# Kernel optimization log

Measured on AMD Instinct MI355X. Metric: run time of the kernel, lower is better.

The kernel has to match this reference:

```python
import jax, jax.numpy as jnp
import numpy as np
import math

DIM = 147      # input feature dim
EMB = 64       # in_dim * head_cnt
M = 32         # int(EMB * kernel_ratio)
EPS_LN = 1e-5
EPS = 1e-8


def layer_norm(x, g, b, eps=EPS_LN):
    mu = jnp.mean(x, axis=-1, keepdims=True)
    var = jnp.mean(jnp.square(x - mu), axis=-1, keepdims=True)
    return (x - mu) * jax.lax.rsqrt(var + eps) * g + b


def prm_exp(x, W_rf):
    # x: [b, t, e], W_rf: [m, e]
    xd = 0.5 * jnp.sum(x * x, axis=-1, keepdims=True)        # [b, t, 1]
    wtx = jnp.einsum('bte,me->btm', x, W_rf)                  # [b, t, m]
    return jnp.exp(wtx - xd) / math.sqrt(M)


def setup_inputs() -> dict:
    key = jax.random.key(0)
    ks = jax.random.split(key, 16)
    B, T = 32, 3136
    s_in = 1.0 / math.sqrt(DIM)
    s_emb = 1.0 / math.sqrt(EMB)
    inp = {
        'x':      jax.random.normal(ks[0], (B, T, DIM), jnp.float32),
        'w_kqv':  jax.random.uniform(ks[1], (3 * EMB, DIM), jnp.float32, -s_in, s_in),
        'b_kqv':  jax.random.uniform(ks[2], (3 * EMB,), jnp.float32, -s_in, s_in),
        'w_proj': jax.random.uniform(ks[3], (EMB, EMB), jnp.float32, -s_emb, s_emb),
        'b_proj': jax.random.uniform(ks[4], (EMB,), jnp.float32, -s_emb, s_emb),
        'g1':     jnp.ones((DIM,), jnp.float32),
        'beta1':  jnp.zeros((DIM,), jnp.float32),
        'g2':     jnp.ones((EMB,), jnp.float32),
        'beta2':  jnp.zeros((EMB,), jnp.float32),
        'w_m1':   jax.random.uniform(ks[5], (EMB, EMB), jnp.float32, -s_emb, s_emb),
        'b_m1':   jax.random.uniform(ks[6], (EMB,), jnp.float32, -s_emb, s_emb),
        'w_m2':   jax.random.uniform(ks[7], (EMB, EMB), jnp.float32, -s_emb, s_emb),
        'b_m2':   jax.random.uniform(ks[8], (EMB,), jnp.float32, -s_emb, s_emb),
        # orthogonal random-feature matrix scaled by sqrt(m) (buffer 'w')
        'W_rf':   jnp.asarray(np.linalg.qr(np.random.RandomState(0).randn(EMB, EMB))[0][:M] * math.sqrt(M), jnp.float32),
    }
    return inp


def reference(x, w_kqv, b_kqv, w_proj, b_proj, g1, beta1, g2, beta2,
              w_m1, b_m1, w_m2, b_m2, W_rf):
    # --- single_attn(norm1(x)) ---
    xn = layer_norm(x, g1, beta1)
    kqv = xn @ w_kqv.T + b_kqv                                  # [b, t, 3e]
    k, q, v = jnp.split(kqv, 3, axis=-1)
    kp = prm_exp(k, W_rf)                                       # [b, t, m]
    qp = prm_exp(q, W_rf)                                       # [b, t, m]
    D = jnp.einsum('btm,bm->bt', qp, kp.sum(axis=1))[..., None]  # [b, t, 1]
    kptv = jnp.einsum('bte,btm->bem', v, kp)                    # [b, e, m]
    y = jnp.einsum('btm,bem->bte', qp, kptv) / (D + EPS)        # [b, t, e]
    y = v + (y @ w_proj.T + b_proj)                             # residual on v
    # --- y + mlp(norm2(y)) ---
    yn = layer_norm(y, g2, beta2)
    h = jax.nn.gelu(yn @ w_m1.T + b_m1, approximate=False)
    out = y + (h @ w_m2.T + b_m2)
    return out
```

## Files before the change

kernel.cpp:

```cpp
#include <hip/hip_runtime.h>
#include <hip/hip_bf16.h>

#define BB 32
#define TT 3136
#define DD 147
#define EE 64
#define MM 32
#define BT (BB*TT)

typedef __hip_bfloat16 bf16;
typedef __attribute__((ext_vector_type(8))) short s8v;
typedef __attribute__((ext_vector_type(4))) float f4v;

__device__ __forceinline__ float b2f(bf16 v){ return __bfloat162float(v); }
__device__ __forceinline__ bf16 f2b(float v){ return __float2bfloat16(v); }
__device__ __forceinline__ unsigned pack2(float a, float b){
  union { bf16 h[2]; unsigned u; } cv; cv.h[0]=f2b(a); cv.h[1]=f2b(b); return cv.u;
}

template<typename T>
__device__ __forceinline__ float cvt1(T v);
template<> __device__ __forceinline__ float cvt1<float>(float v){ return v; }
template<> __device__ __forceinline__ float cvt1<bf16>(bf16 v){ return __bfloat162float(v); }

__device__ __forceinline__ int bf16flag(const void* g1){
  return (*(const unsigned*)g1 == 0x3F803F80u) ? 1 : 0;
}

template<typename T>
__device__ void cvt_body(int idx,
    const T* wkqv, const T* bkqv, const T* Wrf, const T* wproj, const T* bproj,
    const T* g2, const T* be2, const T* wm1, const T* bm1, const T* wm2,
    const T* bm2, const T* g1, const T* be1,
    bf16* Bprep, bf16* WrfB, bf16* w0B, float* bprojF,
    float* g2F, float* be2F, bf16* w1B, float* bm1F, bf16* w2B,
    float* bm2F, float* c2F)
{
  if (idx < 30720){
    int n = idx/160, k = idx - n*160;
    Bprep[idx] = f2b(k < DD ? cvt1(wkqv[n*DD + k]) * cvt1(g1[k]) : 0.f);
    return;
  }
  idx -= 30720;
  if (idx < 2048){ WrfB[idx] = f2b(cvt1(Wrf[idx])); return; }
  idx -= 2048;
  if (idx < 4608){
    int e = idx/72, c = idx - e*72;
    w0B[idx] = f2b(c < 64 ? cvt1(wproj[e*64 + c]) : 0.f); return;
  }
  idx -= 4608;
  if (idx < 64){ bprojF[idx] = cvt1(bproj[idx]); return; }
  idx -= 64;
  if (idx < 64){ g2F[idx] = cvt1(g2[idx]); return; }
  idx -= 64;
  if (idx < 64){ be2F[idx] = cvt1(be2[idx]); return; }
  idx -= 64;
  if (idx < 4608){
    int e = idx/72, c = idx - e*72;
    w1B[idx] = f2b(c < 64 ? cvt1(wm1[e*64 + c]) : 0.f); return;
  }
  idx -= 4608;
  if (idx < 64){ bm1F[idx] = cvt1(bm1[idx]); return; }
  idx -= 64;
  if (idx < 4608){
    int e = idx/72, c = idx - e*72;
    w2B[idx] = f2b(c < 64 ? cvt1(wm2[e*64 + c]) : 0.f); return;
  }
  idx -= 4608;
  if (idx < 64){ bm2F[idx] = cvt1(bm2[idx]); return; }
  idx -= 64;
  if (idx < 192){
    float s = cvt1(bkqv[idx]);
    for (int k=0; k<DD; ++k)
      s = fmaf(cvt1(wkqv[idx*DD + k]), cvt1(be1[k]), s);
    c2F[idx] = s; return;
  }
}

__global__ void k_cvt(const void* wkqv, const void* bkqv, const void* Wrf,
    const void* wproj, const void* bproj, const void* g2, const void* be2,
    const void* wm1, const void* bm1, const void* wm2, const void* bm2,
    const void* g1, const void* be1,
    bf16* Bprep, bf16* WrfB, bf16* w0B, float* bprojF,
    float* g2F, float* be2F, bf16* w1B, float* bm1F, bf16* w2B,
    float* bm2F, float* c2F,
    float* __restrict__ kptvF, float* __restrict__ ksumF)
{
  int idx = blockIdx.x*256 + threadIdx.x;
  if (idx < 65536) kptvF[idx] = 0.f;
  if (idx < 1024)  ksumF[idx] = 0.f;
  if (bf16flag(g1))
    cvt_body<bf16>(idx, (const bf16*)wkqv, (const bf16*)bkqv, (const bf16*)Wrf,
      (const bf16*)wproj, (const bf16*)bproj, (const bf16*)g2, (const bf16*)be2,
      (const bf16*)wm1, (const bf16*)bm1, (const bf16*)wm2, (const bf16*)bm2,
      (const bf16*)g1, (const bf16*)be1,
      Bprep, WrfB, w0B, bprojF, g2F, be2F, w1B, bm1F, w2B, bm2F, c2F);
  else
    cvt_body<float>(idx, (const float*)wkqv, (const float*)bkqv, (const float*)Wrf,
      (const float*)wproj, (const float*)bproj, (const float*)g2, (const float*)be2,
      (const float*)wm1, (const float*)bm1, (const float*)wm2, (const float*)bm2,
      (const float*)g1, (const float*)be1,
      Bprep, WrfB, w0B, bprojF, g2F, be2F, w1B, bm1F, w2B, bm2F, c2F);
}

__global__ __launch_bounds__(256,4) void k_a2(
    const void* __restrict__ x, const void* __restrict__ g1,
    const bf16* __restrict__ Bprep, const float* __restrict__ c2F,
    const bf16* __restrict__ WrfB,
    bf16* __restrict__ qp, bf16* __restrict__ v,
    float* __restrict__ kptvF, float* __restrict__ ksumF)
{
  __shared__ __align__(16) char smem[21504];
  bf16* vT   = (bf16*)smem;
  bf16* kpT  = (bf16*)(smem + 9216);

  int tid = threadIdx.x;
  size_t t0 = (size_t)blockIdx.x*64;
  int b = blockIdx.x / 49;

  int tw = tid>>6, lane = tid&63, quad = lane>>4, r = lane&15;
  int tRow = tw*16 + quad*4;
  char* strip = smem + tw*5376;
  bf16* lin = (bf16*)strip;
  bf16* aS  = (bf16*)strip;
  bf16* kqW = (bf16*)strip;

  if (bf16flag(g1)){
    const uint4* xg = (const uint4*)((const bf16*)x + (t0 + (size_t)tw*16)*DD);
    uint4* xo = (uint4*)lin;
    #pragma unroll
    for (int k=0; k<5; ++k){
      int c = k*64 + lane;
      if (c < 294) xo[c] = xg[c];
    }
  } else {
    const float4* xg = (const float4*)((const float*)x + (t0 + (size_t)tw*16)*DD);
    uint2* xo = (uint2*)lin;
    #pragma unroll
    for (int k=0; k<10; ++k){
      int c = k*64 + lane;
      if (c < 588){
        float4 f = xg[c];
        uint2 u; u.x = pack2(f.x, f.y); u.y = pack2(f.z, f.w);
        xo[c] = u;
      }
    }
  }

  int ti = lane>>2, sl = lane&3;
  const bf16* srow = lin + ti*DD;
  float xv[37];
  float s1 = 0.f, s2 = 0.f;
  #pragma unroll
  for (int j=0; j<37; ++j){
    int e = sl + 4*j;
    float vx = (e < DD) ? b2f(srow[e]) : 0.f;
    xv[j] = vx;
    s1 += vx;
    s2 = fmaf(vx, vx, s2);
  }
  s1 += __shfl_xor(s1,1); s1 += __shfl_xor(s1,2);
  s2 += __shfl_xor(s2,1); s2 += __shfl_xor(s2,2);
  float mu  = s1 * (1.f/147.f);
  float var = s2 * (1.f/147.f) - mu*mu;
  float rn  = rsqrtf(var + 1e-5f);

  bf16* arow = aS + ti*168;
  #pragma unroll
  for (int j=0; j<37; ++j){
    int e = sl + 4*j;
    if (e < DD)       arow[e] = f2b((xv[j]-mu)*rn);
    else if (e == DD) arow[e] = f2b(0.f);
  }
  arow[148+sl] = f2b(0.f); arow[152+sl] = f2b(0.f); arow[156+sl] = f2b(0.f);

  f4v zero = {0.f,0.f,0.f,0.f};

  f4v acc[12];
  #pragma unroll
  for (int nt=0; nt<12; ++nt) acc[nt] = zero;
  const bf16* aBase = aS + r*168 + quad*8;
  const bf16* bBase = &Bprep[r*160 + quad*8];
  #pragma unroll 1
  for (int ks=0; ks<5; ++ks){
    s8v a = *((const s8v*)(aBase + ks*32));
    #pragma unroll
    for (int nt=0; nt<12; ++nt){
      s8v bw = *((const s8v*)(bBase + nt*16*160 + ks*32));
      acc[nt] = __builtin_amdgcn_mfma_f32_16x16x32_bf16(a, bw, acc[nt], 0,0,0);
    }
  }

  float c2v[12];
  #pragma unroll
  for (int nt=0; nt<12; ++nt) c2v[nt] = c2F[nt*16 + r];

  float vv[4][4];
  #pragma unroll
  for (int nt=8; nt<12; ++nt){
    #pragma unroll
    for (int reg=0; reg<4; ++reg){
      vv[nt-8][reg] = acc[nt][reg] + c2v[nt];
      v[(t0 + tRow + reg)*64 + (nt-8)*16 + r] = f2b(vv[nt-8][reg]);
    }
  }

  float kq[8][4];
  #pragma unroll
  for (int nt=0; nt<8; ++nt)
    #pragma unroll
    for (int reg=0; reg<4; ++reg)
      kq[nt][reg] = acc[nt][reg] + c2v[nt];

  #pragma unroll
  for (int nt=0; nt<8; ++nt)
    #pragma unroll
    for (int reg=0; reg<4; ++reg)
      kqW[(quad*4+reg)*136 + nt*16 + r] = f2b(kq[nt][reg]);

  float xdk[4], xdq[4];
  #pragma unroll
  for (int reg=0; reg<4; ++reg){
    float sk = 0.f, sq = 0.f;
    #pragma unroll
    for (int nt=0; nt<4; ++nt){
      sk = fmaf(kq[nt][reg],   kq[nt][reg],   sk);
      sq = fmaf(kq[nt+4][reg], kq[nt+4][reg], sq);
    }
    #pragma unroll
    for (int off=1; off<16; off<<=1){
      sk += __shfl_xor(sk, off);
      sq += __shfl_xor(sq, off);
    }
    xdk[reg] = 0.5f*sk;
    xdq[reg] = 0.5f*sq;
  }

  f4v accP[2] = {zero, zero}, accQ[2] = {zero, zero};
  #pragma unroll
  for (int ks=0; ks<2; ++ks){
    s8v ak = *((const s8v*)&kqW[r*136 + ks*32 + quad*8]);
    s8v aq = *((const s8v*)&kqW[r*136 + 64 + ks*32 + quad*8]);
    #pragma unroll
    for (int nt=0; nt<2; ++nt){
      s8v wf = *((const s8v*)&WrfB[(nt*16+r)*64 + ks*32 + quad*8]);
      accP[nt] = __builtin_amdgcn_mfma_f32_16x16x32_bf16(ak, wf, accP[nt], 0,0,0);
      accQ[nt] = __builtin_amdgcn_mfma_f32_16x16x32_bf16(aq, wf, accQ[nt], 0,0,0);
    }
  }
  float kpv[2][4];
  #pragma unroll
  for (int nt=0; nt<2; ++nt){
    #pragma unroll
    for (int reg=0; reg<4; ++reg){
      size_t gt = t0 + tRow + reg;
      kpv[nt][reg] = expf(accP[nt][reg] - xdk[reg]) * 0.17677669529663687f;
      qp[gt*32 + nt*16 + r] = f2b(expf(accQ[nt][reg] - xdq[reg]) * 0.17677669529663687f);
    }
  }
  __syncthreads();

  #pragma unroll
  for (int nt=0; nt<4; ++nt){
    *((unsigned*)&vT[(nt*16+r)*72 + tRow])     = pack2(vv[nt][0], vv[nt][1]);
    *((unsigned*)&vT[(nt*16+r)*72 + tRow + 2]) = pack2(vv[nt][2], vv[nt][3]);
  }
  #pragma unroll
  for (int nt=0; nt<2; ++nt){
    *((unsigned*)&kpT[(nt*16+r)*72 + tRow])     = pack2(kpv[nt][0], kpv[nt][1]);
    *((unsigned*)&kpT[(nt*16+r)*72 + tRow + 2]) = pack2(kpv[nt][2], kpv[nt][3]);
  }

  float ks0 = kpv[0][0]+kpv[0][1]+kpv[0][2]+kpv[0][3];
  float ks1 = kpv[1][0]+kpv[1][1]+kpv[1][2]+kpv[1][3];
  ks0 += __shfl_xor(ks0, 16); ks0 += __shfl_xor(ks0, 32);
  ks1 += __shfl_xor(ks1, 16); ks1 += __shfl_xor(ks1, 32);
  if (lane < 16){
    atomicAdd(&ksumF[b*32 + r],      ks0);
    atomicAdd(&ksumF[b*32 + 16 + r], ks1);
  }
  __syncthreads();

  f4v accKV[2] = {zero, zero};
  #pragma unroll
  for (int kh=0; kh<2; ++kh){
    s8v av = *((const s8v*)&vT[(tw*16+r)*72 + kh*32 + quad*8]);
    #pragma unroll
    for (int nt=0; nt<2; ++nt){
      s8v bk = *((const s8v*)&kpT[(nt*16+r)*72 + kh*32 + quad*8]);
      accKV[nt] = __builtin_amdgcn_mfma_f32_16x16x32_bf16(av, bk, accKV[nt], 0,0,0);
    }
  }
  float* dst = kptvF + b*2048;
  #pragma unroll
  for (int nt=0; nt<2; ++nt)
    #pragma unroll
    for (int reg=0; reg<4; ++reg)
      atomicAdd(&dst[(tw*16 + quad*4 + reg)*32 + nt*16 + r], accKV[nt][reg]);
}

__global__ __launch_bounds__(256,2) void k_b(
    const bf16* __restrict__ qp, const bf16* __restrict__ v,
    const float* __restrict__ kptvF, const float* __restrict__ ksumF,
    const bf16* __restrict__ w0B, const float* __restrict__ bprojF,
    const float* __restrict__ g2F, const float* __restrict__ be2F,
    const bf16* __restrict__ w1B, const float* __restrict__ bm1F,
    const bf16* __restrict__ w2B, const float* __restrict__ bm2F,
    const void* __restrict__ g1, void* __restrict__ outp)
{
  __shared__ __align__(16) bf16 qpS[64*40];
  __shared__ __align__(16) bf16 kvS[64*40];
  __shared__ __align__(16) bf16 w0S[64*72];
  __shared__ __align__(16) bf16 w1S[64*72];
  __shared__ __align__(16) bf16 w2S[64*72];
  __shared__ __align__(16) bf16 vS[64*72];
  __shared__ __align__(16) bf16 stA[64*72];
  __shared__ __align__(16) bf16 stB[64*72];
  __shared__ float ksS[32];
  __shared__ float bpS[64], b1S[64], b2S[64], gS[64], btS[64];

  int flag = bf16flag(g1);
  int tid = threadIdx.x;
  int b = blockIdx.y;
  int gt0 = b*TT + blockIdx.x*64;

  {
    int t = tid>>2, q = tid&3;
    uint4 u = ((const uint4*)(qp + (size_t)gt0*32))[tid];
    *((uint4*)&qpS[t*40 + q*8]) = u;
  }
  for (int i=tid; i<512; i+=256){
    int e = i>>3, q = i&7;
    float4 f = ((const float4*)(kptvF + b*2048))[i];
    union { bf16 h[4]; uint2 u; } cv;
    cv.h[0]=f2b(f.x); cv.h[1]=f2b(f.y); cv.h[2]=f2b(f.z); cv.h[3]=f2b(f.w);
    *((uint2*)&kvS[e*40 + q*4]) = cv.u;
  }
  for (int i=tid; i<512; i+=256){
    int t = i>>3, q = i&7;
    uint4 u = ((const uint4*)(v + (size_t)gt0*64))[i];
    *((uint4*)&vS[t*72 + q*8]) = u;
  }
  for (int i=tid; i<576; i+=256) ((uint4*)w0S)[i] = ((const uint4*)w0B)[i];
  for (int i=tid; i<576; i+=256) ((uint4*)w1S)[i] = ((const uint4*)w1B)[i];
  for (int i=tid; i<576; i+=256) ((uint4*)w2S)[i] = ((const uint4*)w2B)[i];
  if (tid<32) ksS[tid] = ksumF[b*32+tid];
  if (tid<64){
    bpS[tid]=bprojF[tid]; b1S[tid]=bm1F[tid]; b2S[tid]=bm2F[tid];
    gS[tid]=g2F[tid]; btS[tid]=be2F[tid];
  }
  __syncthreads();

  int tw = tid>>6, lane = tid&63, quad = lane>>4, r = lane&15;
  int tRow = tw*16 + quad*4;
  f4v zero = {0.f,0.f,0.f,0.f};

  float dpart;
  {
    int ti = lane>>2, sl = lane&3;
    const bf16* qrow = &qpS[(tw*16+ti)*40];
    float s = 0.f;
    #pragma unroll
    for (int m=0; m<8; ++m) s = fmaf(b2f(qrow[sl*8+m]), ksS[sl*8+m], s);
    s += __shfl_xor(s,1); s += __shfl_xor(s,2);
    dpart = s;
  }
  float Dinv[4];
  #pragma unroll
  for (int reg=0; reg<4; ++reg){
    float d = __shfl(dpart, (lane & 0x30) + 4*reg);
    Dinv[reg] = 1.f/(d + 1e-8f);
  }

  f4v accA[4];
  {
    s8v aq = *((const s8v*)&qpS[(tw*16+r)*40 + quad*8]);
    #pragma unroll
    for (int nt=0; nt<4; ++nt){
      s8v bk = *((const s8v*)&kvS[(nt*16+r)*40 + quad*8]);
      accA[nt] = __builtin_amdgcn_mfma_f32_16x16x32_bf16(aq, bk, zero, 0,0,0);
    }
  }

  #pragma unroll
  for (int nt=0; nt<4; ++nt)
    #pragma unroll
    for (int reg=0; reg<4; ++reg)
      stA[(tRow+reg)*72 + nt*16 + r] = f2b(accA[nt][reg]*Dinv[reg]);

  f4v accY[4] = {zero, zero, zero, zero};
  #pragma unroll
  for (int kh=0; kh<2; ++kh){
    s8v ay = *((const s8v*)&stA[(tw*16+r)*72 + kh*32 + quad*8]);
    #pragma unroll
    for (int nt=0; nt<4; ++nt){
      s8v bw = *((const s8v*)&w0S[(nt*16+r)*72 + kh*32 + quad*8]);
      accY[nt] = __builtin_amdgcn_mfma_f32_16x16x32_bf16(ay, bw, accY[nt], 0,0,0);
    }
  }
  float y[4][4];
  #pragma unroll
  for (int nt=0; nt<4; ++nt){
    int e = nt*16 + r;
    float bp = bpS[e];
    #pragma unroll
    for (int reg=0; reg<4; ++reg)
      y[nt][reg] = accY[nt][reg] + b2f(vS[(tRow+reg)*72 + e]) + bp;
  }

  float mu[4], rs[4];
  #pragma unroll
  for (int reg=0; reg<4; ++reg){
    float s = y[0][reg]+y[1][reg]+y[2][reg]+y[3][reg];
    #pragma unroll
    for (int off=1; off<16; off<<=1) s += __shfl_xor(s, off);
    mu[reg] = s * (1.f/64.f);
  }
  #pragma unroll
  for (int reg=0; reg<4; ++reg){
    float d2 = 0.f;
    #pragma unroll
    for (int nt=0; nt<4; ++nt){ float d = y[nt][reg]-mu[reg]; d2 = fmaf(d,d,d2); }
    #pragma unroll
    for (int off=1; off<16; off<<=1) d2 += __shfl_xor(d2, off);
    rs[reg] = rsqrtf(d2*(1.f/64.f) + 1e-5f);
  }
  #pragma unroll
  for (int nt=0; nt<4; ++nt){
    int e = nt*16 + r;
    float g = gS[e], be = btS[e];
    #pragma unroll
    for (int reg=0; reg<4; ++reg)
      stB[(tRow+reg)*72 + e] = f2b((y[nt][reg]-mu[reg])*rs[reg]*g + be);
  }

  f4v accH[4] = {zero, zero, zero, zero};
  #pragma unroll
  for (int kh=0; kh<2; ++kh){
    s8v ah = *((const s8v*)&stB[(tw*16+r)*72 + kh*32 + quad*8]);
    #pragma unroll
    for (int nt=0; nt<4; ++nt){
      s8v bw = *((const s8v*)&w1S[(nt*16+r)*72 + kh*32 + quad*8]);
      accH[nt] = __builtin_amdgcn_mfma_f32_16x16x32_bf16(ah, bw, accH[nt], 0,0,0);
    }
  }
  #pragma unroll
  for (int nt=0; nt<4; ++nt){
    int e = nt*16 + r;
    float b1 = b1S[e];
    #pragma unroll
    for (int reg=0; reg<4; ++reg){
      float h = accH[nt][reg] + b1;
      h = 0.5f*h*(1.f + erff(h*0.70710678118654752f));
      stA[(tRow+reg)*72 + e] = f2b(h);
    }
  }

  f4v accO[4] = {zero, zero, zero, zero};
  #pragma unroll
  for (int kh=0; kh<2; ++kh){
    s8v ao = *((const s8v*)&stA[(tw*16+r)*72 + kh*32 + quad*8]);
    #pragma unroll
    for (int nt=0; nt<4; ++nt){
      s8v bw = *((const s8v*)&w2S[(nt*16+r)*72 + kh*32 + quad*8]);
      accO[nt] = __builtin_amdgcn_mfma_f32_16x16x32_bf16(ao, bw, accO[nt], 0,0,0);
    }
  }
  if (flag){
    bf16* o = (bf16*)outp;
    #pragma unroll
    for (int nt=0; nt<4; ++nt){
      int e = nt*16 + r;
      float b2 = b2S[e];
      #pragma unroll
      for (int reg=0; reg<4; ++reg)
        o[(size_t)(gt0 + tRow + reg)*64 + e] = f2b(y[nt][reg] + accO[nt][reg] + b2);
    }
  } else {
    float* o = (float*)outp;
    #pragma unroll
    for (int nt=0; nt<4; ++nt){
      int e = nt*16 + r;
      float b2 = b2S[e];
      #pragma unroll
      for (int reg=0; reg<4; ++reg)
        o[(size_t)(gt0 + tRow + reg)*64 + e] = y[nt][reg] + accO[nt][reg] + b2;
    }
  }
}

extern "C" void kernel_launch(void* const* d_in, const int* in_sizes, int n_in,
                              void* d_out, int out_size, void* d_ws, size_t ws_size,
                              hipStream_t stream){
  const void* x    = d_in[0];
  const void* wkqv = d_in[1];
  const void* bkqv = d_in[2];
  const void* wproj= d_in[3];
  const void* bproj= d_in[4];
  const void* g1   = d_in[5];
  const void* be1  = d_in[6];
  const void* g2   = d_in[7];
  const void* be2  = d_in[8];
  const void* wm1  = d_in[9];
  const void* bm1  = d_in[10];
  const void* wm2  = d_in[11];
  const void* bm2  = d_in[12];
  const void* Wrf  = d_in[13];

  char* ws = (char*)d_ws;
  bf16*  Bprep = (bf16*) (ws + 256);
  bf16*  WrfB  = (bf16*) (ws + 62464);
  bf16*  w0B   = (bf16*) (ws + 66560);
  float* bprojF= (float*)(ws + 82944);
  float* g2F   = (float*)(ws + 83200);
  float* be2F  = (float*)(ws + 83456);
  bf16*  w1B   = (bf16*) (ws + 83712);
  float* bm1F  = (float*)(ws + 100096);
  bf16*  w2B   = (bf16*) (ws + 100352);
  float* bm2F  = (float*)(ws + 116736);
  float* c2F   = (float*)(ws + 118784);
  float* kptvF = (float*)(ws + 32231424);
  float* ksumF = (float*)(ws + 32493568);
  bf16*  qp    = (bf16*) (ws + 32497664);
  bf16*  v     = (bf16*) (ws + 38920192);

  k_cvt<<<256, 256, 0, stream>>>(wkqv, bkqv, Wrf, wproj, bproj, g2, be2,
      wm1, bm1, wm2, bm2, g1, be1,
      Bprep, WrfB, w0B, bprojF, g2F, be2F, w1B, bm1F, w2B, bm2F,
      c2F, kptvF, ksumF);
  k_a2<<<BT/64, 256, 0, stream>>>(x, g1, Bprep, c2F, WrfB,
      qp, v, kptvF, ksumF);
  k_b<<<dim3(TT/64, BB), 256, 0, stream>>>(qp, v, kptvF, ksumF,
      w0B, bprojF, g2F, be2F, w1B, bm1F, w2B, bm2F, g1, d_out);
}
```

Before: 199.7 us.

## Read MLP weights from global, shrink k_b LDS, raise occupancy, parallelize bias fold

In k_b, the three 64x64 weight matrices are no longer copied into shared memory; MFMA operands are loaded straight from global (L1/L2-cached) memory. The separate stB staging buffer is dropped in favour of reusing stA, which cuts LDS per block substantially, and launch bounds are raised for k_b and k_a2 to allow more resident blocks. The c2F bias-fold precompute now uses a 64-lane wave reduction per output instead of a serial loop in one thread. The trade-off is more global/cache traffic for the weight reads in exchange for higher occupancy, plus a possible reuse hazard on stA between waves, though each wave touches only its own rows.

```diff
diff --git a/kernel.cpp b/kernel.cpp
--- a/kernel.cpp
+++ b/kernel.cpp
@@ -69,11 +69,16 @@
   idx -= 4608;
   if (idx < 64){ bm2F[idx] = cvt1(bm2[idx]); return; }
   idx -= 64;
-  if (idx < 192){
-    float s = cvt1(bkqv[idx]);
-    for (int k=0; k<DD; ++k)
-      s = fmaf(cvt1(wkqv[idx*DD + k]), cvt1(be1[k]), s);
-    c2F[idx] = s; return;
+  if (idx < 12288){
+    int n = idx>>6, ln = idx&63;
+    float s = cvt1(wkqv[n*DD + ln])    * cvt1(be1[ln])
+            + cvt1(wkqv[n*DD + 64+ln]) * cvt1(be1[64+ln]);
+    if (ln < DD-128)
+      s = fmaf(cvt1(wkqv[n*DD + 128+ln]), cvt1(be1[128+ln]), s);
+    #pragma unroll
+    for (int off=32; off; off>>=1) s += __shfl_xor(s, off);
+    if (ln == 0) c2F[n] = s + cvt1(bkqv[n]);
+    return;
   }
 }
 
@@ -103,7 +108,7 @@
       Bprep, WrfB, w0B, bprojF, g2F, be2F, w1B, bm1F, w2B, bm2F, c2F);
 }
 
-__global__ __launch_bounds__(256,4) void k_a2(
+__global__ __launch_bounds__(256,6) void k_a2(
     const void* __restrict__ x, const void* __restrict__ g1,
     const bf16* __restrict__ Bprep, const float* __restrict__ c2F,
     const bf16* __restrict__ WrfB,
@@ -299,7 +304,7 @@
       atomicAdd(&dst[(tw*16 + quad*4 + reg)*32 + nt*16 + r], accKV[nt][reg]);
 }
 
-__global__ __launch_bounds__(256,2) void k_b(
+__global__ __launch_bounds__(256,4) void k_b(
     const bf16* __restrict__ qp, const bf16* __restrict__ v,
     const float* __restrict__ kptvF, const float* __restrict__ ksumF,
     const bf16* __restrict__ w0B, const float* __restrict__ bprojF,
@@ -310,12 +315,8 @@
 {
   __shared__ __align__(16) bf16 qpS[64*40];
   __shared__ __align__(16) bf16 kvS[64*40];
-  __shared__ __align__(16) bf16 w0S[64*72];
-  __shared__ __align__(16) bf16 w1S[64*72];
-  __shared__ __align__(16) bf16 w2S[64*72];
   __shared__ __align__(16) bf16 vS[64*72];
   __shared__ __align__(16) bf16 stA[64*72];
-  __shared__ __align__(16) bf16 stB[64*72];
   __shared__ float ksS[32];
   __shared__ float bpS[64], b1S[64], b2S[64], gS[64], btS[64];
 
@@ -341,9 +342,6 @@
     uint4 u = ((const uint4*)(v + (size_t)gt0*64))[i];
     *((uint4*)&vS[t*72 + q*8]) = u;
   }
-  for (int i=tid; i<576; i+=256) ((uint4*)w0S)[i] = ((const uint4*)w0B)[i];
-  for (int i=tid; i<576; i+=256) ((uint4*)w1S)[i] = ((const uint4*)w1B)[i];
-  for (int i=tid; i<576; i+=256) ((uint4*)w2S)[i] = ((const uint4*)w2B)[i];
   if (tid<32) ksS[tid] = ksumF[b*32+tid];
   if (tid<64){
     bpS[tid]=bprojF[tid]; b1S[tid]=bm1F[tid]; b2S[tid]=bm2F[tid];
@@ -394,7 +392,7 @@
     s8v ay = *((const s8v*)&stA[(tw*16+r)*72 + kh*32 + quad*8]);
     #pragma unroll
     for (int nt=0; nt<4; ++nt){
-      s8v bw = *((const s8v*)&w0S[(nt*16+r)*72 + kh*32 + quad*8]);
+      s8v bw = *((const s8v*)&w0B[(nt*16+r)*72 + kh*32 + quad*8]);
       accY[nt] = __builtin_amdgcn_mfma_f32_16x16x32_bf16(ay, bw, accY[nt], 0,0,0);
     }
   }
@@ -431,16 +429,16 @@
     float g = gS[e], be = btS[e];
     #pragma unroll
     for (int reg=0; reg<4; ++reg)
-      stB[(tRow+reg)*72 + e] = f2b((y[nt][reg]-mu[reg])*rs[reg]*g + be);
+      stA[(tRow+reg)*72 + e] = f2b((y[nt][reg]-mu[reg])*rs[reg]*g + be);
   }
 
   f4v accH[4] = {zero, zero, zero, zero};
   #pragma unroll
   for (int kh=0; kh<2; ++kh){
-    s8v ah = *((const s8v*)&stB[(tw*16+r)*72 + kh*32 + quad*8]);
-    #pragma unroll
-    for (int nt=0; nt<4; ++nt){
-      s8v bw = *((const s8v*)&w1S[(nt*16+r)*72 + kh*32 + quad*8]);
+    s8v ah = *((const s8v*)&stA[(tw*16+r)*72 + kh*32 + quad*8]);
+    #pragma unroll
+    for (int nt=0; nt<4; ++nt){
+      s8v bw = *((const s8v*)&w1B[(nt*16+r)*72 + kh*32 + quad*8]);
       accH[nt] = __builtin_amdgcn_mfma_f32_16x16x32_bf16(ah, bw, accH[nt], 0,0,0);
     }
   }
@@ -462,7 +460,7 @@
     s8v ao = *((const s8v*)&stA[(tw*16+r)*72 + kh*32 + quad*8]);
     #pragma unroll
     for (int nt=0; nt<4; ++nt){
-      s8v bw = *((const s8v*)&w2S[(nt*16+r)*72 + kh*32 + quad*8]);
+      s8v bw = *((const s8v*)&w2B[(nt*16+r)*72 + kh*32 + quad*8]);
       accO[nt] = __builtin_amdgcn_mfma_f32_16x16x32_bf16(ao, bw, accO[nt], 0,0,0);
     }
   }
```

Result: no change. 196.0 us (-1.9%).
